# Kernel tuning notes

Hardware: AMD Instinct MI355X
Metric: run time of the kernel (lower is better)

The kernel has to match this reference:

```python
import jax, jax.numpy as jnp
import numpy as np

D_STATE = 32

def _layernorm(x, g, b, eps=1e-5):
    m = jnp.mean(x, -1, keepdims=True)
    v = jnp.mean((x - m) ** 2, -1, keepdims=True)
    return (x - m) * jax.lax.rsqrt(v + eps) * g + b

def _mlp(x, W1, b1, W2, b2):
    return jax.nn.relu(x @ W1 + b1) @ W2 + b2

def _mamba_block(x, Win, Wconv, bconv, Wxproj, Wdt, bdt, Alog, Dp, Wout):
    Bsz, T, _ = x.shape
    d_inner = Wconv.shape[0]
    dt_rank = Wdt.shape[0]
    xz = x @ Win                                   # [B,T,2*d_inner]
    xi, res = jnp.split(xz, 2, axis=-1)
    K = Wconv.shape[1]
    xp = jnp.pad(xi, ((0, 0), (K - 1, 0), (0, 0)))  # causal depthwise conv
    xi = sum(xp[:, k:k + T, :] * Wconv[:, k] for k in range(K)) + bconv
    xi = jax.nn.silu(xi)
    xdbl = xi @ Wxproj                              # [B,T,dt_rank+2*ds]
    dtr = xdbl[..., :dt_rank]
    Bm = xdbl[..., dt_rank:dt_rank + D_STATE]
    Cm = xdbl[..., dt_rank + D_STATE:]
    dt = jax.nn.softplus(dtr @ Wdt + bdt)           # [B,T,d_inner]
    A = -jnp.exp(Alog)                              # [d_inner, ds]

    def step(h, inp):
        dt_t, B_t, C_t, x_t = inp                   # [B,di],[B,ds],[B,ds],[B,di]
        dA = jnp.exp(dt_t[:, :, None] * A)          # [B,di,ds]
        dBx = (dt_t * x_t)[:, :, None] * B_t[:, None, :]
        h = dA * h + dBx
        return h, jnp.einsum('bds,bs->bd', h, C_t)

    h0 = jnp.zeros((Bsz, d_inner, D_STATE), xi.dtype)
    _, ys = jax.lax.scan(step, h0, (jnp.swapaxes(dt, 0, 1), jnp.swapaxes(Bm, 0, 1),
                                    jnp.swapaxes(Cm, 0, 1), jnp.swapaxes(xi, 0, 1)))
    y = jnp.swapaxes(ys, 0, 1) + xi * Dp
    y = y * jax.nn.silu(res)
    return y @ Wout

def _dynamics(z, Win, Wconv, bconv, Wxproj, Wdt, bdt, Alog, Dp, Wout, gamma, beta):
    out = z
    for i in range(Win.shape[0]):  # 2 stacked residual Mamba blocks
        out = out + _mamba_block(out, Win[i], Wconv[i], bconv[i], Wxproj[i],
                                 Wdt[i], bdt[i], Alog[i], Dp[i], Wout[i])
    return _layernorm(out, gamma, beta)

def setup_inputs():
    key = jax.random.key(0)
    Bz, T, IN, D, DI, DTR, K, NB = 8, 1024, 32, 64, 128, 4, 4, 2
    ks = iter(jax.random.split(key, 32))
    n = lambda shape, s=0.02: jax.random.normal(next(ks), shape, jnp.float32) * s
    return {
        'x': jax.random.normal(next(ks), (Bz, T, IN), jnp.float32),
        'We1': n((IN, 64)), 'be1': jnp.zeros((64,)),
        'We2': n((64, D)), 'be2': jnp.zeros((D,)),
        'Wd1': n((D, 64)), 'bd1': jnp.zeros((64,)),
        'Wd2': n((64, IN)), 'bd2': jnp.zeros((IN,)),
        'Win': n((NB, D, 2 * DI)),
        'Wconv': n((NB, DI, K), 0.1), 'bconv': jnp.zeros((NB, DI)),
        'Wxproj': n((NB, DI, DTR + 2 * D_STATE)),
        'Wdt': n((NB, DTR, DI), 0.1), 'bdt': jnp.full((NB, DI), -4.0),
        'Alog': jnp.tile(jnp.log(jnp.arange(1.0, 33.0)), (NB, DI, 1)),
        'Dparam': jnp.ones((NB, DI)),
        'Wout': n((NB, DI, D)),
        'gamma': jnp.ones((D,)), 'beta': jnp.zeros((D,)),
        'pred_len': 4,
    }

def reference(x, We1, be1, We2, be2, Wd1, bd1, Wd2, bd2, Win, Wconv, bconv,
              Wxproj, Wdt, bdt, Alog, Dparam, Wout, gamma, beta, pred_len):
    z = _mlp(x, We1, be1, We2, be2)
    x_rec = _mlp(z, Wd1, bd1, Wd2, bd2)
    dyn = lambda u: _dynamics(u, Win, Wconv, bconv, Wxproj, Wdt, bdt,
                              Alog, Dparam, Wout, gamma, beta)
    z_dyn = dyn(z)
    x_dyn = _mlp(z_dyn, Wd1, bd1, Wd2, bd2)
    x_pred = None
    if pred_len > 0:
        T = z.shape[1]
        curr = z
        preds = []
        for _ in range(pred_len):
            z_next = dyn(curr[:, -T:, :])[:, -1:, :]
            preds.append(z_next)
            curr = jnp.concatenate([curr, z_next], axis=1)
        x_pred = _mlp(jnp.concatenate(preds, axis=1), Wd1, bd1, Wd2, bd2)
    return (x_rec, x_dyn, x_pred, z, z_dyn)
```

## Files before the change

kernel.cpp:

```cpp
#include <hip/hip_runtime.h>

#define BSZ 8
#define TLEN 1024
#define DM 64
#define DI 128
#define DS 32
#define NCHUNK 16
#define CLEN 64
#define GEXT 1028

__device__ __forceinline__ float siluf(float x) { return x / (1.f + expf(-x)); }
__device__ __forceinline__ float softplusf(float x) { return (x > 20.f) ? x : log1pf(expf(x)); }

__global__ __launch_bounds__(256) void enc_xrec_kernel(
    const float* __restrict__ x,
    const float* __restrict__ We1, const float* __restrict__ be1,
    const float* __restrict__ We2, const float* __restrict__ be2,
    const float* __restrict__ Wd1, const float* __restrict__ bd1,
    const float* __restrict__ Wd2, const float* __restrict__ bd2,
    float* __restrict__ z, float* __restrict__ x_rec)
{
  __shared__ float s_x[16*32];
  __shared__ float s_h1[16*64];
  __shared__ float s_z[16*64];
  __shared__ float s_h2[16*64];
  const int tid = threadIdx.x;
  const int t0 = blockIdx.x * 16;
  s_x[tid]       = x[(size_t)t0*32 + tid];
  s_x[tid + 256] = x[(size_t)t0*32 + tid + 256];
  __syncthreads();
  const int j = tid & 63, tg = tid >> 6;
  {
    float w[32];
    #pragma unroll
    for (int k = 0; k < 32; k++) w[k] = We1[k*64 + j];
    #pragma unroll
    for (int q = 0; q < 4; q++) {
      int t = tg*4 + q;
      float a = be1[j];
      #pragma unroll
      for (int k = 0; k < 32; k++) a = fmaf(s_x[t*32 + k], w[k], a);
      s_h1[t*64 + j] = fmaxf(a, 0.f);
    }
  }
  __syncthreads();
  {
    float w[64];
    #pragma unroll
    for (int k = 0; k < 64; k++) w[k] = We2[k*64 + j];
    #pragma unroll
    for (int q = 0; q < 4; q++) {
      int t = tg*4 + q;
      float a = be2[j];
      #pragma unroll
      for (int k = 0; k < 64; k++) a = fmaf(s_h1[t*64 + k], w[k], a);
      s_z[t*64 + j] = a;
      z[(size_t)(t0 + t)*64 + j] = a;
    }
  }
  __syncthreads();
  {
    float w[64];
    #pragma unroll
    for (int k = 0; k < 64; k++) w[k] = Wd1[k*64 + j];
    #pragma unroll
    for (int q = 0; q < 4; q++) {
      int t = tg*4 + q;
      float a = bd1[j];
      #pragma unroll
      for (int k = 0; k < 64; k++) a = fmaf(s_z[t*64 + k], w[k], a);
      s_h2[t*64 + j] = fmaxf(a, 0.f);
    }
  }
  __syncthreads();
  {
    const int c = tid & 31, tg2 = tid >> 5;
    float w[64];
    #pragma unroll
    for (int k = 0; k < 64; k++) w[k] = Wd2[k*32 + c];
    #pragma unroll
    for (int q = 0; q < 2; q++) {
      int t = tg2*2 + q;
      float a = bd2[c];
      #pragma unroll
      for (int k = 0; k < 64; k++) a = fmaf(s_h2[t*64 + k], w[k], a);
      x_rec[(size_t)(t0 + t)*32 + c] = a;
    }
  }
}

__global__ __launch_bounds__(256) void dec2_kernel(
    const float* __restrict__ za, const float* __restrict__ zb,
    const float* __restrict__ W1, const float* __restrict__ b1,
    const float* __restrict__ W2, const float* __restrict__ b2,
    float* __restrict__ outa, float* __restrict__ outb)
{
  __shared__ float s_z[16*64];
  __shared__ float s_h[16*64];
  const int tid = threadIdx.x;
  const float* src; float* dst; int t0;
  if (blockIdx.x < 512) { src = za; dst = outa; t0 = blockIdx.x * 16; }
  else                  { src = zb; dst = outb; t0 = (blockIdx.x - 512) * 16; }
  #pragma unroll
  for (int u = 0; u < 4; u++) s_z[tid + u*256] = src[(size_t)t0*64 + tid + u*256];
  __syncthreads();
  const int j = tid & 63, tg = tid >> 6;
  {
    float w[64];
    #pragma unroll
    for (int k = 0; k < 64; k++) w[k] = W1[k*64 + j];
    #pragma unroll
    for (int q = 0; q < 4; q++) {
      int t = tg*4 + q;
      float a = b1[j];
      #pragma unroll
      for (int k = 0; k < 64; k++) a = fmaf(s_z[t*64 + k], w[k], a);
      s_h[t*64 + j] = fmaxf(a, 0.f);
    }
  }
  __syncthreads();
  {
    const int c = tid & 31, tg2 = tid >> 5;
    float w[64];
    #pragma unroll
    for (int k = 0; k < 64; k++) w[k] = W2[k*32 + c];
    #pragma unroll
    for (int q = 0; q < 2; q++) {
      int t = tg2*2 + q;
      float a = b2[c];
      #pragma unroll
      for (int k = 0; k < 64; k++) a = fmaf(s_h[t*64 + k], w[k], a);
      dst[(size_t)(t0 + t)*32 + c] = a;
    }
  }
}

__global__ __launch_bounds__(256,4) void pre_kernel(
    const float* __restrict__ in, int in_stride,
    const float* __restrict__ Win, const float* __restrict__ Wconv, const float* __restrict__ bconv,
    const float* __restrict__ Wxproj, const float* __restrict__ Wdt, const float* __restrict__ bdt,
    float* __restrict__ xibuf, float* __restrict__ resgbuf,
    float2* __restrict__ ddbuf, float* __restrict__ Bbuf, float* __restrict__ Cbuf,
    float* __restrict__ xzout)
{
  __shared__ float s_xi[8*128];
  __shared__ float s_dtr[8*4];
  const int tid = threadIdx.x;
  const int b  = blockIdx.x >> 7;
  const int t0 = (blockIdx.x & 127) * 8;

  const float* rowp[11];
  #pragma unroll
  for (int r = 0; r < 11; r++) {
    int tg = t0 - 3 + r;
    rowp[r] = (tg >= 0) ? in + ((size_t)b*in_stride + tg)*DM : in;
  }

  float acc[11];
  #pragma unroll
  for (int r = 0; r < 11; r++) acc[r] = 0.f;

  if (t0 > 0) {
    #pragma unroll
    for (int k4 = 0; k4 < 16; k4++) {
      float w0 = Win[(k4*4+0)*256 + tid];
      float w1 = Win[(k4*4+1)*256 + tid];
      float w2 = Win[(k4*4+2)*256 + tid];
      float w3 = Win[(k4*4+3)*256 + tid];
      #pragma unroll
      for (int r = 0; r < 11; r++) {
        float4 xv = *(const float4*)(rowp[r] + k4*4);
        acc[r] = fmaf(xv.x, w0, acc[r]);
        acc[r] = fmaf(xv.y, w1, acc[r]);
        acc[r] = fmaf(xv.z, w2, acc[r]);
        acc[r] = fmaf(xv.w, w3, acc[r]);
      }
    }
  } else {
    #pragma unroll
    for (int k4 = 0; k4 < 16; k4++) {
      float w0 = Win[(k4*4+0)*256 + tid];
      float w1 = Win[(k4*4+1)*256 + tid];
      float w2 = Win[(k4*4+2)*256 + tid];
      float w3 = Win[(k4*4+3)*256 + tid];
      #pragma unroll
      for (int r = 3; r < 11; r++) {
        float4 xv = *(const float4*)(rowp[r] + k4*4);
        acc[r] = fmaf(xv.x, w0, acc[r]);
        acc[r] = fmaf(xv.y, w1, acc[r]);
        acc[r] = fmaf(xv.z, w2, acc[r]);
        acc[r] = fmaf(xv.w, w3, acc[r]);
      }
    }
  }

  if (tid < 128) {
    float4 wc = *(const float4*)&Wconv[tid*4];
    float bc = bconv[tid];
    #pragma unroll
    for (int tau = 0; tau < 8; tau++) {
      float v = bc;
      v = fmaf(acc[tau+0], wc.x, v);
      v = fmaf(acc[tau+1], wc.y, v);
      v = fmaf(acc[tau+2], wc.z, v);
      v = fmaf(acc[tau+3], wc.w, v);
      float xiv = siluf(v);
      s_xi[tau*128 + tid] = xiv;
      xibuf[((size_t)b*TLEN + t0 + tau)*DI + tid] = xiv;
      xzout[((size_t)b*GEXT + t0 + tau)*128 + tid] = acc[tau+3];
    }
  } else {
    int d = tid - 128;
    #pragma unroll
    for (int tau = 0; tau < 8; tau++)
      resgbuf[((size_t)b*TLEN + t0 + tau)*DI + d] = siluf(acc[tau+3]);
  }
  __syncthreads();
  {
    const int wv = tid >> 6, c = tid & 63;
    float a0 = 0.f, a1 = 0.f;
    const float4* x0 = (const float4*)&s_xi[(wv*2+0)*128];
    const float4* x1 = (const float4*)&s_xi[(wv*2+1)*128];
    #pragma unroll 4
    for (int k4 = 0; k4 < 32; k4++) {
      float wq0 = Wxproj[(k4*4+0)*68 + 4 + c];
      float wq1 = Wxproj[(k4*4+1)*68 + 4 + c];
      float wq2 = Wxproj[(k4*4+2)*68 + 4 + c];
      float wq3 = Wxproj[(k4*4+3)*68 + 4 + c];
      float4 v0 = x0[k4], v1 = x1[k4];
      a0 = fmaf(v0.x,wq0, fmaf(v0.y,wq1, fmaf(v0.z,wq2, fmaf(v0.w,wq3, a0))));
      a1 = fmaf(v1.x,wq0, fmaf(v1.y,wq1, fmaf(v1.z,wq2, fmaf(v1.w,wq3, a1))));
    }
    size_t tb = (size_t)b*TLEN + t0 + wv*2;
    if (c < 32) {
      Bbuf[(tb+0)*DS + c] = a0; Bbuf[(tb+1)*DS + c] = a1;
    } else {
      int cc = c - 32;
      Cbuf[(tb+0)*DS + cc] = a0; Cbuf[(tb+1)*DS + cc] = a1;
    }
  }
  if (tid < 32) {
    int tau = tid >> 2, cc = tid & 3;
    float a = 0.f;
    const float4* xx = (const float4*)&s_xi[tau*128];
    #pragma unroll 4
    for (int k4 = 0; k4 < 32; k4++) {
      float4 v = xx[k4];
      a = fmaf(v.x, Wxproj[(k4*4+0)*68 + cc], a);
      a = fmaf(v.y, Wxproj[(k4*4+1)*68 + cc], a);
      a = fmaf(v.z, Wxproj[(k4*4+2)*68 + cc], a);
      a = fmaf(v.w, Wxproj[(k4*4+3)*68 + cc], a);
    }
    s_dtr[tau*4 + cc] = a;
  }
  __syncthreads();
  #pragma unroll
  for (int u = 0; u < 4; u++) {
    int i = tid + u*256;
    int tau = i >> 7, d = i & 127;
    float a = bdt[d];
    #pragma unroll
    for (int r = 0; r < 4; r++) a = fmaf(s_dtr[tau*4 + r], Wdt[r*128 + d], a);
    float dtv = softplusf(a);
    ddbuf[((size_t)b*TLEN + t0 + tau)*DI + d] = make_float2(dtv, dtv * s_xi[i]);
  }
}

#define BSWZ(row3) (((row3)&3)<<1)

__device__ __forceinline__ int xcd_wid_4096() {
  return (blockIdx.x >> 3) | ((blockIdx.x & 7) << 9);
}

__global__ __launch_bounds__(128) void scan1_kernel(
    const float2* __restrict__ ddbuf, const float* __restrict__ Bbuf,
    const float* __restrict__ Alog, float2* __restrict__ hc)
{
  __shared__ float2 s_dd[4][CLEN];
  __shared__ float  s_Bt[32][68];
  const int tid = threadIdx.x;
  const int ch = tid >> 5, s = tid & 31;
  const int wid = xcd_wid_4096();
  const int dg = wid & 31;
  const int c  = (wid >> 5) & 15;
  const int b  = wid >> 9;
  const int d0 = dg * 4;
  const float A = -__expf(Alog[(d0 + ch)*DS + s]);
  const float2* ddg = ddbuf + ((size_t)b*TLEN + c*CLEN)*DI + d0;
  const float*  Bg  = Bbuf  + ((size_t)b*TLEN + c*CLEN)*DS;
  {
    int t = tid >> 1, half = tid & 1;
    float4 rdd = *(const float4*)((const float*)(ddg + (size_t)t*DI) + half*4);
    s_dd[2*half+0][t] = make_float2(rdd.x, rdd.y);
    s_dd[2*half+1][t] = make_float2(rdd.z, rdd.w);
    #pragma unroll
    for (int j = 0; j < 4; j++) {
      int q = tid + 128*j; int tt = q >> 3, k4 = q & 7;
      float4 rB = *(const float4*)(Bg + tt*DS + k4*4);
      int cp = (((tt>>2) ^ BSWZ(k4>>1)) << 2) + (tt & 3);
      s_Bt[k4*4+0][cp] = rB.x; s_Bt[k4*4+1][cp] = rB.y;
      s_Bt[k4*4+2][cp] = rB.z; s_Bt[k4*4+3][cp] = rB.w;
    }
  }
  __syncthreads();
  float h = 0.f, dts = 0.f;
  const float4* dd4 = (const float4*)&s_dd[ch][0];
  const float4* bt4 = (const float4*)&s_Bt[s][0];
  const int swr = BSWZ(s>>3);
  #pragma unroll
  for (int j = 0; j < 8; j++) {
    float4 e0 = dd4[4*j+0], e1 = dd4[4*j+1], e2 = dd4[4*j+2], e3 = dd4[4*j+3];
    float4 bb0 = bt4[(2*j)^swr], bb1 = bt4[(2*j+1)^swr];
    h = fmaf(__expf(e0.x*A), h, e0.y*bb0.x);
    h = fmaf(__expf(e0.z*A), h, e0.w*bb0.y);
    h = fmaf(__expf(e1.x*A), h, e1.y*bb0.z);
    h = fmaf(__expf(e1.z*A), h, e1.w*bb0.w);
    h = fmaf(__expf(e2.x*A), h, e2.y*bb1.x);
    h = fmaf(__expf(e2.z*A), h, e2.w*bb1.y);
    h = fmaf(__expf(e3.x*A), h, e3.y*bb1.z);
    h = fmaf(__expf(e3.z*A), h, e3.w*bb1.w);
    dts += (e0.x + e0.z) + (e1.x + e1.z) + (e2.x + e2.z) + (e3.x + e3.z);
  }
  int o = ((b*NCHUNK + c)*DI + d0 + ch)*DS + s;
  hc[o] = make_float2(h, __expf(A*dts));
}

__global__ __launch_bounds__(128) void scan3_kernel(
    const float2* __restrict__ ddbuf, const float* __restrict__ Bbuf, const float* __restrict__ Cbuf,
    const float* __restrict__ Alog, const float2* __restrict__ hc, float* __restrict__ ysbuf,
    float* __restrict__ hout)
{
  __shared__ float2 s_dd[4][CLEN];
  __shared__ float  s_Bt[32][68];
  __shared__ float  s_Ct[32][68];
  __shared__ float  s_p[128][33];
  const int tid = threadIdx.x;
  const int ch = tid >> 5, s = tid & 31;
  const int wid = xcd_wid_4096();
  const int dg = wid & 31;
  const int c  = (wid >> 5) & 15;
  const int b  = wid >> 9;
  const int d0 = dg * 4;
  const float A = -__expf(Alog[(d0 + ch)*DS + s]);
  const float2* ddg = ddbuf + ((size_t)b*TLEN + c*CLEN)*DI + d0;
  const float*  Bg  = Bbuf  + ((size_t)b*TLEN + c*CLEN)*DS;
  const float*  Cg  = Cbuf  + ((size_t)b*TLEN + c*CLEN)*DS;

  const int ob = (d0 + ch)*DS + s;
  float2 v[15];
  #pragma unroll
  for (int q = 0; q < 15; q++) v[q] = hc[(size_t)(b*NCHUNK + q)*4096 + ob];

  {
    int t = tid >> 1, half = tid & 1;
    float4 rdd = *(const float4*)((const float*)(ddg + (size_t)t*DI) + half*4);
    s_dd[2*half+0][t] = make_float2(rdd.x, rdd.y);
    s_dd[2*half+1][t] = make_float2(rdd.z, rdd.w);
    #pragma unroll
    for (int j = 0; j < 4; j++) {
      int q = tid + 128*j; int tt = q >> 3, k4 = q & 7;
      float4 rB = *(const float4*)(Bg + tt*DS + k4*4);
      float4 rC = *(const float4*)(Cg + tt*DS + k4*4);
      int cp = (((tt>>2) ^ BSWZ(k4>>1)) << 2) + (tt & 3);
      s_Bt[k4*4+0][cp] = rB.x; s_Bt[k4*4+1][cp] = rB.y;
      s_Bt[k4*4+2][cp] = rB.z; s_Bt[k4*4+3][cp] = rB.w;
      s_Ct[k4*4+0][cp] = rC.x; s_Ct[k4*4+1][cp] = rC.y;
      s_Ct[k4*4+2][cp] = rC.z; s_Ct[k4*4+3][cp] = rC.w;
    }
  }
  float h = 0.f;
  #pragma unroll
  for (int q = 0; q < 15; q++)
    if (q < c) h = fmaf(v[q].y, h, v[q].x);
  __syncthreads();

  const float4* dd4 = (const float4*)&s_dd[ch][0];
  const float4* bt4 = (const float4*)&s_Bt[s][0];
  const float4* ct4 = (const float4*)&s_Ct[s][0];
  const int swr = BSWZ(s>>3);
  float* pr = &s_p[tid][0];
  #pragma unroll
  for (int half = 0; half < 2; half++) {
    #pragma unroll
    for (int j = 0; j < 4; j++) {
      const int jj = half*4 + j;
      float4 e0 = dd4[4*jj+0], e1 = dd4[4*jj+1], e2 = dd4[4*jj+2], e3 = dd4[4*jj+3];
      float4 bb0 = bt4[(2*jj)^swr], bb1 = bt4[(2*jj+1)^swr];
      float4 cc0 = ct4[(2*jj)^swr], cc1 = ct4[(2*jj+1)^swr];
      h = fmaf(__expf(e0.x*A), h, e0.y*bb0.x); pr[8*j+0] = h*cc0.x;
      h = fmaf(__expf(e0.z*A), h, e0.w*bb0.y); pr[8*j+1] = h*cc0.y;
      h = fmaf(__expf(e1.x*A), h, e1.y*bb0.z); pr[8*j+2] = h*cc0.z;
      h = fmaf(__expf(e1.z*A), h, e1.w*bb0.w); pr[8*j+3] = h*cc0.w;
      h = fmaf(__expf(e2.x*A), h, e2.y*bb1.x); pr[8*j+4] = h*cc1.x;
      h = fmaf(__expf(e2.z*A), h, e2.w*bb1.y); pr[8*j+5] = h*cc1.y;
      h = fmaf(__expf(e3.x*A), h, e3.y*bb1.z); pr[8*j+6] = h*cc1.z;
      h = fmaf(__expf(e3.z*A), h, e3.w*bb1.w); pr[8*j+7] = h*cc1.w;
    }
    __syncthreads();
    {
      const int ch2 = tid & 3;
      const int tq  = tid >> 2;
      float a = 0.f;
      #pragma unroll
      for (int s2 = 0; s2 < 32; s2++) a += s_p[ch2*32 + s2][tq];
      ysbuf[(size_t)(b*TLEN + c*CLEN + half*32 + tq)*DI + d0 + ch2] = a;
    }
    __syncthreads();
  }
  if (c == 15) hout[(size_t)(b*DI + d0 + ch)*DS + s] = h;
}

__global__ __launch_bounds__(256,4) void post_kernel(
    const float* __restrict__ ysbuf, const float* __restrict__ xibuf, const float* __restrict__ resgbuf,
    const float* __restrict__ Dp, const float* __restrict__ Wout,
    const float* __restrict__ basebuf, int base_stride,
    float* __restrict__ curg, float* __restrict__ zdyn, float* __restrict__ predz,
    const float* __restrict__ gamma, const float* __restrict__ beta, int mode)
{
  __shared__ float s_y[8*128];
  const int tid = threadIdx.x;
  const int b  = blockIdx.x >> 7;
  const int t0 = (blockIdx.x & 127) * 8;
  #pragma unroll
  for (int u = 0; u < 4; u++) {
    int i = tid + u*256;
    size_t g = (size_t)(b*TLEN + t0)*DI + i;
    s_y[i] = (ysbuf[g] + xibuf[g]*Dp[i & 127]) * resgbuf[g];
  }
  __syncthreads();
  #pragma unroll
  for (int u = 0; u < 2; u++) {
    int i = tid + u*256;
    int tau = i >> 6, c = i & 63;
    float a = 0.f;
    const float4* yy = (const float4*)&s_y[tau*128];
    #pragma unroll 4
    for (int k4 = 0; k4 < 32; k4++) {
      float4 vv = yy[k4];
      a = fmaf(vv.x, Wout[(k4*4+0)*64 + c], a);
      a = fmaf(vv.y, Wout[(k4*4+1)*64 + c], a);
      a = fmaf(vv.z, Wout[(k4*4+2)*64 + c], a);
      a = fmaf(vv.w, Wout[(k4*4+3)*64 + c], a);
    }
    float base = basebuf[((size_t)b*base_stride + t0 + tau)*DM + c];
    float val = base + a;
    if (mode == 0) {
      curg[((size_t)b*GEXT + t0 + tau)*DM + c] = val;
    } else {
      float sum = val;
      #pragma unroll
      for (int m = 1; m < 64; m <<= 1) sum += __shfl_xor(sum, m);
      float mean = sum * (1.f/64.f);
      float dv = val - mean;
      float vs = dv*dv;
      #pragma unroll
      for (int m = 1; m < 64; m <<= 1) vs += __shfl_xor(vs, m);
      float oln = dv * rsqrtf(vs*(1.f/64.f) + 1e-5f) * gamma[c] + beta[c];
      zdyn[(size_t)(b*TLEN + t0 + tau)*DM + c] = oln;
      if (t0 + tau == TLEN-1) predz[(size_t)(b*4 + 0)*DM + c] = oln;
    }
  }
}

__device__ __forceinline__ void mamba_token(
    int tid, int b, int gn, const float* __restrict__ s_in,
    float* __restrict__ xzg, float* __restrict__ hbuf,
    const float* __restrict__ Win, const float* __restrict__ Wcv, const float* __restrict__ bcv,
    const float* __restrict__ Wxp, const float* __restrict__ Wdt, const float* __restrict__ bdt,
    const float* __restrict__ Al, const float* __restrict__ Dpp, const float* __restrict__ Wo,
    float* __restrict__ s_xz, float* __restrict__ s_xi, float* __restrict__ s_rg,
    float* __restrict__ s_dt, float* __restrict__ s_B, float* __restrict__ s_C,
    float* __restrict__ s_dtr, float* __restrict__ s_yp, float* __restrict__ s_y,
    float* __restrict__ s_ssm)
{
  {
    float a = 0.f;
    #pragma unroll
    for (int k = 0; k < 64; k++) a = fmaf(s_in[k], Win[k*256 + tid], a);
    s_xz[tid] = a;
  }
  __syncthreads();
  if (tid < 128) {
    xzg[((size_t)b*GEXT + gn)*128 + tid] = s_xz[tid];
    float acc = bcv[tid];
    acc = fmaf(xzg[((size_t)b*GEXT + gn-3)*128 + tid], Wcv[tid*4+0], acc);
    acc = fmaf(xzg[((size_t)b*GEXT + gn-2)*128 + tid], Wcv[tid*4+1], acc);
    acc = fmaf(xzg[((size_t)b*GEXT + gn-1)*128 + tid], Wcv[tid*4+2], acc);
    acc = fmaf(s_xz[tid], Wcv[tid*4+3], acc);
    s_xi[tid] = siluf(acc);
    s_rg[tid] = siluf(s_xz[128 + tid]);
  }
  __syncthreads();
  if (tid < 68) {
    float a = 0.f;
    #pragma unroll 4
    for (int k = 0; k < 128; k++) a = fmaf(s_xi[k], Wxp[k*68 + tid], a);
    if (tid < 4)       s_dtr[tid] = a;
    else if (tid < 36) s_B[tid-4] = a;
    else               s_C[tid-36] = a;
  }
  __syncthreads();
  if (tid < 128) {
    float a = bdt[tid];
    #pragma unroll
    for (int r = 0; r < 4; r++) a = fmaf(s_dtr[r], Wdt[r*128 + tid], a);
    s_dt[tid] = softplusf(a);
  }
  __syncthreads();
  {
    int d = tid >> 1, sh = (tid & 1) * 16;
    float dtd = s_dt[d], dtxd = dtd * s_xi[d];
    float yp = 0.f;
    #pragma unroll
    for (int q = 0; q < 16; q++) {
      int s = sh + q;
      size_t oo = (size_t)(b*DI + d)*DS + s;
      float A = -__expf(Al[d*DS + s]);
      float h = hbuf[oo];
      h = fmaf(__expf(dtd*A), h, dtxd*s_B[s]);
      hbuf[oo] = h;
      yp = fmaf(s_C[s], h, yp);
    }
    s_yp[(tid & 1)*128 + d] = yp;
  }
  __syncthreads();
  if (tid < 128) s_y[tid] = ((s_yp[tid] + s_yp[128 + tid]) + s_xi[tid]*Dpp[tid]) * s_rg[tid];
  __syncthreads();
  if (tid < 64) {
    float a = 0.f;
    #pragma unroll 4
    for (int k = 0; k < 128; k++) a = fmaf(s_y[k], Wo[k*64 + tid], a);
    s_ssm[tid] = a;
  }
  __syncthreads();
}

__global__ __launch_bounds__(256) void ext2_kernel(
    int p,
    float* __restrict__ predz, float* __restrict__ curg,
    float* __restrict__ xz0, float* __restrict__ xz1,
    float* __restrict__ hbuf0, float* __restrict__ hbuf1,
    const float* __restrict__ Win0, const float* __restrict__ Wcv0, const float* __restrict__ bcv0,
    const float* __restrict__ Wxp0, const float* __restrict__ Wdt0, const float* __restrict__ bdt0,
    const float* __restrict__ Al0, const float* __restrict__ Dp0, const float* __restrict__ Wo0,
    const float* __restrict__ Win1, const float* __restrict__ Wcv1, const float* __restrict__ bcv1,
    const float* __restrict__ Wxp1, const float* __restrict__ Wdt1, const float* __restrict__ bdt1,
    const float* __restrict__ Al1, const float* __restrict__ Dp1, const float* __restrict__ Wo1,
    const float* __restrict__ gamma, const float* __restrict__ beta)
{
  __shared__ float s_in[64], s_cg[64], s_ssm[64];
  __shared__ float s_xz[256], s_yp[256];
  __shared__ float s_xi[128], s_rg[128], s_dt[128], s_y[128];
  __shared__ float s_B[32], s_C[32], s_dtr[4];
  const int tid = threadIdx.x;
  const int b = blockIdx.x;
  const int gn = 1023 + p;

  if (tid < 64) s_in[tid] = predz[(size_t)(b*4 + p-1)*DM + tid];
  __syncthreads();
  mamba_token(tid, b, gn, s_in, xz0, hbuf0, Win0, Wcv0, bcv0, Wxp0, Wdt0, bdt0,
              Al0, Dp0, Wo0, s_xz, s_xi, s_rg, s_dt, s_B, s_C, s_dtr, s_yp, s_y, s_ssm);
  if (tid < 64) {
    float cg = s_in[tid] + s_ssm[tid];
    curg[((size_t)b*GEXT + gn)*DM + tid] = cg;
    s_cg[tid] = cg;
  }
  __syncthreads();
  if (tid < 64) s_in[tid] = s_cg[tid];
  __syncthreads();
  mamba_token(tid, b, gn, s_in, xz1, hbuf1, Win1, Wcv1, bcv1, Wxp1, Wdt1, bdt1,
              Al1, Dp1, Wo1, s_xz, s_xi, s_rg, s_dt, s_B, s_C, s_dtr, s_yp, s_y, s_ssm);
  if (tid < 64) {
    float val = s_cg[tid] + s_ssm[tid];
    float sum = val;
    #pragma unroll
    for (int m = 1; m < 64; m <<= 1) sum += __shfl_xor(sum, m);
    float mean = sum * (1.f/64.f);
    float dv = val - mean;
    float vs = dv*dv;
    #pragma unroll
    for (int m = 1; m < 64; m <<= 1) vs += __shfl_xor(vs, m);
    float oln = dv * rsqrtf(vs*(1.f/64.f) + 1e-5f) * gamma[tid] + beta[tid];
    predz[(size_t)(b*4 + p)*DM + tid] = oln;
  }
}

extern "C" void kernel_launch(void* const* d_in, const int* in_sizes, int n_in,
                              void* d_out, int out_size, void* d_ws, size_t ws_size,
                              hipStream_t stream)
{
  (void)in_sizes; (void)n_in; (void)out_size; (void)ws_size;
  const float* x     = (const float*)d_in[0];
  const float* We1   = (const float*)d_in[1];
  const float* be1   = (const float*)d_in[2];
  const float* We2   = (const float*)d_in[3];
  const float* be2   = (const float*)d_in[4];
  const float* Wd1   = (const float*)d_in[5];
  const float* bd1   = (const float*)d_in[6];
  const float* Wd2   = (const float*)d_in[7];
  const float* bd2   = (const float*)d_in[8];
  const float* Win   = (const float*)d_in[9];
  const float* Wconv = (const float*)d_in[10];
  const float* bconv = (const float*)d_in[11];
  const float* Wxp   = (const float*)d_in[12];
  const float* Wdt   = (const float*)d_in[13];
  const float* bdt   = (const float*)d_in[14];
  const float* Alog  = (const float*)d_in[15];
  const float* Dp    = (const float*)d_in[16];
  const float* Wout  = (const float*)d_in[17];
  const float* gamma = (const float*)d_in[18];
  const float* beta  = (const float*)d_in[19];

  float* o      = (float*)d_out;
  float* x_rec  = o;
  float* x_dyn  = o + 262144;
  float* x_pred = o + 524288;
  float* z      = o + 525312;
  float* zdyn   = o + 1049600;

  float* w      = (float*)d_ws;
  float* xi0    = w;
  float* resg0  = xi0   + 1048576;
  float2* dd0   = (float2*)(resg0 + 1048576);
  float* Bb0    = resg0 + 1048576 + 2097152;
  float* Cb0    = Bb0   + 262144;
  float* xi1    = Cb0   + 262144;
  float* resg1  = xi1   + 1048576;
  float2* dd1   = (float2*)(resg1 + 1048576);
  float* Bb1    = resg1 + 1048576 + 2097152;
  float* Cb1    = Bb1   + 262144;
  float* ys     = Cb1   + 262144;
  float2* hc    = (float2*)(ys + 1048576);
  float* predz  = ys + 1048576 + 1048576;
  float* xz0    = predz + 2048;
  float* xz1    = xz0   + 1052672;
  float* curg   = xz1   + 1052672;
  float* hbuf0  = curg  + 526336;
  float* hbuf1  = hbuf0 + 32768;

  const float* Win0 = Win,   *Win1 = Win + 64*256;
  const float* Wcv0 = Wconv, *Wcv1 = Wconv + 128*4;
  const float* bcv0 = bconv, *bcv1 = bconv + 128;
  const float* Wxp0 = Wxp,   *Wxp1 = Wxp + 128*68;
  const float* Wdt0 = Wdt,   *Wdt1 = Wdt + 4*128;
  const float* bdt0 = bdt,   *bdt1 = bdt + 128;
  const float* Al0  = Alog,  *Al1  = Alog + 128*32;
  const float* Dp0  = Dp,    *Dp1  = Dp + 128;
  const float* Wo0  = Wout,  *Wo1  = Wout + 128*64;

  enc_xrec_kernel<<<dim3(512), dim3(256), 0, stream>>>(x, We1, be1, We2, be2, Wd1, bd1, Wd2, bd2, z, x_rec);

  pre_kernel<<<dim3(1024), dim3(256), 0, stream>>>(z, TLEN,
                                                   Win0, Wcv0, bcv0, Wxp0, Wdt0, bdt0,
                                                   xi0, resg0, dd0, Bb0, Cb0, xz0);
  scan1_kernel<<<dim3(4096), dim3(128), 0, stream>>>(dd0, Bb0, Al0, hc);
  scan3_kernel<<<dim3(4096), dim3(128), 0, stream>>>(dd0, Bb0, Cb0, Al0, hc, ys, hbuf0);
  post_kernel<<<dim3(1024), dim3(256), 0, stream>>>(ys, xi0, resg0, Dp0, Wo0,
                                                    z, TLEN, curg,
                                                    (float*)nullptr, (float*)nullptr,
                                                    (const float*)nullptr, (const float*)nullptr, 0);

  pre_kernel<<<dim3(1024), dim3(256), 0, stream>>>(curg, GEXT,
                                                   Win1, Wcv1, bcv1, Wxp1, Wdt1, bdt1,
                                                   xi1, resg1, dd1, Bb1, Cb1, xz1);
  scan1_kernel<<<dim3(4096), dim3(128), 0, stream>>>(dd1, Bb1, Al1, hc);
  scan3_kernel<<<dim3(4096), dim3(128), 0, stream>>>(dd1, Bb1, Cb1, Al1, hc, ys, hbuf1);
  post_kernel<<<dim3(1024), dim3(256), 0, stream>>>(ys, xi1, resg1, Dp1, Wo1,
                                                    curg, GEXT, (float*)nullptr,
                                                    zdyn, predz, gamma, beta, 1);

  for (int p = 1; p <= 3; p++) {
    ext2_kernel<<<dim3(8), dim3(256), 0, stream>>>(p, predz, curg, xz0, xz1, hbuf0, hbuf1,
        Win0, Wcv0, bcv0, Wxp0, Wdt0, bdt0, Al0, Dp0, Wo0,
        Win1, Wcv1, bcv1, Wxp1, Wdt1, bdt1, Al1, Dp1, Wo1,
        gamma, beta);
  }

  dec2_kernel<<<dim3(514), dim3(256), 0, stream>>>(zdyn, predz, Wd1, bd1, Wd2, bd2, x_dyn, x_pred);
}
```

Baseline: 242.3 us.

## Fuse decoder MLP into post kernel and merge prediction steps into one kernel

The x_dyn decoder MLP now runs inside the second post_kernel on the layernormed tokens already held in shared memory, so the separate dec2 kernel and its re-read of zdyn go away. The three per-step ext2 launches become one ext_all_kernel that loops over prediction steps, keeps predicted tokens in shared memory, and decodes x_pred at the end. This cuts five launches to two fewer kernels and removes global round trips. In exchange post_kernel uses more shared memory and registers, which could lower occupancy, and the x_pred decode runs on only 8 blocks.

```diff
diff --git a/kernel.cpp b/kernel.cpp
--- a/kernel.cpp
+++ b/kernel.cpp
@@ -85,52 +85,6 @@
       #pragma unroll
       for (int k = 0; k < 64; k++) a = fmaf(s_h2[t*64 + k], w[k], a);
       x_rec[(size_t)(t0 + t)*32 + c] = a;
-    }
-  }
-}
-
-__global__ __launch_bounds__(256) void dec2_kernel(
-    const float* __restrict__ za, const float* __restrict__ zb,
-    const float* __restrict__ W1, const float* __restrict__ b1,
-    const float* __restrict__ W2, const float* __restrict__ b2,
-    float* __restrict__ outa, float* __restrict__ outb)
-{
-  __shared__ float s_z[16*64];
-  __shared__ float s_h[16*64];
-  const int tid = threadIdx.x;
-  const float* src; float* dst; int t0;
-  if (blockIdx.x < 512) { src = za; dst = outa; t0 = blockIdx.x * 16; }
-  else                  { src = zb; dst = outb; t0 = (blockIdx.x - 512) * 16; }
-  #pragma unroll
-  for (int u = 0; u < 4; u++) s_z[tid + u*256] = src[(size_t)t0*64 + tid + u*256];
-  __syncthreads();
-  const int j = tid & 63, tg = tid >> 6;
-  {
-    float w[64];
-    #pragma unroll
-    for (int k = 0; k < 64; k++) w[k] = W1[k*64 + j];
-    #pragma unroll
-    for (int q = 0; q < 4; q++) {
-      int t = tg*4 + q;
-      float a = b1[j];
-      #pragma unroll
-      for (int k = 0; k < 64; k++) a = fmaf(s_z[t*64 + k], w[k], a);
-      s_h[t*64 + j] = fmaxf(a, 0.f);
-    }
-  }
-  __syncthreads();
-  {
-    const int c = tid & 31, tg2 = tid >> 5;
-    float w[64];
-    #pragma unroll
-    for (int k = 0; k < 64; k++) w[k] = W2[k*32 + c];
-    #pragma unroll
-    for (int q = 0; q < 2; q++) {
-      int t = tg2*2 + q;
-      float a = b2[c];
-      #pragma unroll
-      for (int k = 0; k < 64; k++) a = fmaf(s_h[t*64 + k], w[k], a);
-      dst[(size_t)(t0 + t)*32 + c] = a;
     }
   }
 }
@@ -415,9 +369,14 @@
     const float* __restrict__ Dp, const float* __restrict__ Wout,
     const float* __restrict__ basebuf, int base_stride,
     float* __restrict__ curg, float* __restrict__ zdyn, float* __restrict__ predz,
-    const float* __restrict__ gamma, const float* __restrict__ beta, int mode)
+    const float* __restrict__ gamma, const float* __restrict__ beta,
+    const float* __restrict__ Wd1, const float* __restrict__ bd1,
+    const float* __restrict__ Wd2, const float* __restrict__ bd2,
+    float* __restrict__ xdyn, int mode)
 {
   __shared__ float s_y[8*128];
+  __shared__ float s_z[8*64];
+  __shared__ float s_h[8*64];
   const int tid = threadIdx.x;
   const int b  = blockIdx.x >> 7;
   const int t0 = (blockIdx.x & 127) * 8;
@@ -457,7 +416,42 @@
       for (int m = 1; m < 64; m <<= 1) vs += __shfl_xor(vs, m);
       float oln = dv * rsqrtf(vs*(1.f/64.f) + 1e-5f) * gamma[c] + beta[c];
       zdyn[(size_t)(b*TLEN + t0 + tau)*DM + c] = oln;
+      s_z[tau*64 + c] = oln;
       if (t0 + tau == TLEN-1) predz[(size_t)(b*4 + 0)*DM + c] = oln;
+    }
+  }
+  if (mode == 1) {
+    __syncthreads();
+    #pragma unroll
+    for (int u = 0; u < 2; u++) {
+      int i = tid + u*256;
+      int t = i >> 6, j = i & 63;
+      float a = bd1[j];
+      const float4* zz = (const float4*)&s_z[t*64];
+      #pragma unroll 4
+      for (int k4 = 0; k4 < 16; k4++) {
+        float4 zv = zz[k4];
+        a = fmaf(zv.x, Wd1[(k4*4+0)*64 + j], a);
+        a = fmaf(zv.y, Wd1[(k4*4+1)*64 + j], a);
+        a = fmaf(zv.z, Wd1[(k4*4+2)*64 + j], a);
+        a = fmaf(zv.w, Wd1[(k4*4+3)*64 + j], a);
+      }
+      s_h[i] = fmaxf(a, 0.f);
+    }
+    __syncthreads();
+    {
+      int t = tid >> 5, c = tid & 31;
+      float a = bd2[c];
+      const float4* hh = (const float4*)&s_h[t*64];
+      #pragma unroll 4
+      for (int k4 = 0; k4 < 16; k4++) {
+        float4 hv = hh[k4];
+        a = fmaf(hv.x, Wd2[(k4*4+0)*32 + c], a);
+        a = fmaf(hv.y, Wd2[(k4*4+1)*32 + c], a);
+        a = fmaf(hv.z, Wd2[(k4*4+2)*32 + c], a);
+        a = fmaf(hv.w, Wd2[(k4*4+3)*32 + c], a);
+      }
+      xdyn[(size_t)(b*TLEN + t0 + t)*32 + c] = a;
     }
   }
 }
@@ -535,8 +529,7 @@
   __syncthreads();
 }
 
-__global__ __launch_bounds__(256) void ext2_kernel(
-    int p,
+__global__ __launch_bounds__(256) void ext_all_kernel(
     float* __restrict__ predz, float* __restrict__ curg,
     float* __restrict__ xz0, float* __restrict__ xz1,
     float* __restrict__ hbuf0, float* __restrict__ hbuf1,
@@ -546,42 +539,83 @@
     const float* __restrict__ Win1, const float* __restrict__ Wcv1, const float* __restrict__ bcv1,
     const float* __restrict__ Wxp1, const float* __restrict__ Wdt1, const float* __restrict__ bdt1,
     const float* __restrict__ Al1, const float* __restrict__ Dp1, const float* __restrict__ Wo1,
-    const float* __restrict__ gamma, const float* __restrict__ beta)
+    const float* __restrict__ gamma, const float* __restrict__ beta,
+    const float* __restrict__ Wd1, const float* __restrict__ bd1,
+    const float* __restrict__ Wd2, const float* __restrict__ bd2,
+    float* __restrict__ x_pred)
 {
   __shared__ float s_in[64], s_cg[64], s_ssm[64];
   __shared__ float s_xz[256], s_yp[256];
   __shared__ float s_xi[128], s_rg[128], s_dt[128], s_y[128];
   __shared__ float s_B[32], s_C[32], s_dtr[4];
+  __shared__ float s_pz[4][64];
+  __shared__ float s_h[4][64];
   const int tid = threadIdx.x;
   const int b = blockIdx.x;
-  const int gn = 1023 + p;
-
-  if (tid < 64) s_in[tid] = predz[(size_t)(b*4 + p-1)*DM + tid];
-  __syncthreads();
-  mamba_token(tid, b, gn, s_in, xz0, hbuf0, Win0, Wcv0, bcv0, Wxp0, Wdt0, bdt0,
-              Al0, Dp0, Wo0, s_xz, s_xi, s_rg, s_dt, s_B, s_C, s_dtr, s_yp, s_y, s_ssm);
-  if (tid < 64) {
-    float cg = s_in[tid] + s_ssm[tid];
-    curg[((size_t)b*GEXT + gn)*DM + tid] = cg;
-    s_cg[tid] = cg;
-  }
-  __syncthreads();
-  if (tid < 64) s_in[tid] = s_cg[tid];
-  __syncthreads();
-  mamba_token(tid, b, gn, s_in, xz1, hbuf1, Win1, Wcv1, bcv1, Wxp1, Wdt1, bdt1,
-              Al1, Dp1, Wo1, s_xz, s_xi, s_rg, s_dt, s_B, s_C, s_dtr, s_yp, s_y, s_ssm);
-  if (tid < 64) {
-    float val = s_cg[tid] + s_ssm[tid];
-    float sum = val;
-    #pragma unroll
-    for (int m = 1; m < 64; m <<= 1) sum += __shfl_xor(sum, m);
-    float mean = sum * (1.f/64.f);
-    float dv = val - mean;
-    float vs = dv*dv;
-    #pragma unroll
-    for (int m = 1; m < 64; m <<= 1) vs += __shfl_xor(vs, m);
-    float oln = dv * rsqrtf(vs*(1.f/64.f) + 1e-5f) * gamma[tid] + beta[tid];
-    predz[(size_t)(b*4 + p)*DM + tid] = oln;
+
+  if (tid < 64) s_pz[0][tid] = predz[(size_t)(b*4 + 0)*DM + tid];
+  __syncthreads();
+
+  for (int p = 1; p <= 3; p++) {
+    const int gn = 1023 + p;
+    if (tid < 64) s_in[tid] = s_pz[p-1][tid];
+    __syncthreads();
+    mamba_token(tid, b, gn, s_in, xz0, hbuf0, Win0, Wcv0, bcv0, Wxp0, Wdt0, bdt0,
+                Al0, Dp0, Wo0, s_xz, s_xi, s_rg, s_dt, s_B, s_C, s_dtr, s_yp, s_y, s_ssm);
+    if (tid < 64) {
+      float cg = s_in[tid] + s_ssm[tid];
+      curg[((size_t)b*GEXT + gn)*DM + tid] = cg;
+      s_cg[tid] = cg;
+      s_in[tid] = cg;
+    }
+    __syncthreads();
+    mamba_token(tid, b, gn, s_in, xz1, hbuf1, Win1, Wcv1, bcv1, Wxp1, Wdt1, bdt1,
+                Al1, Dp1, Wo1, s_xz, s_xi, s_rg, s_dt, s_B, s_C, s_dtr, s_yp, s_y, s_ssm);
+    if (tid < 64) {
+      float val = s_cg[tid] + s_ssm[tid];
+      float sum = val;
+      #pragma unroll
+      for (int m = 1; m < 64; m <<= 1) sum += __shfl_xor(sum, m);
+      float mean = sum * (1.f/64.f);
+      float dv = val - mean;
+      float vs = dv*dv;
+      #pragma unroll
+      for (int m = 1; m < 64; m <<= 1) vs += __shfl_xor(vs, m);
+      float oln = dv * rsqrtf(vs*(1.f/64.f) + 1e-5f) * gamma[tid] + beta[tid];
+      predz[(size_t)(b*4 + p)*DM + tid] = oln;
+      s_pz[p][tid] = oln;
+    }
+    __syncthreads();
+  }
+
+  {
+    int t = tid >> 6, j = tid & 63;
+    float a = bd1[j];
+    const float4* zz = (const float4*)&s_pz[t][0];
+    #pragma unroll 4
+    for (int k4 = 0; k4 < 16; k4++) {
+      float4 zv = zz[k4];
+      a = fmaf(zv.x, Wd1[(k4*4+0)*64 + j], a);
+      a = fmaf(zv.y, Wd1[(k4*4+1)*64 + j], a);
+      a = fmaf(zv.z, Wd1[(k4*4+2)*64 + j], a);
+      a = fmaf(zv.w, Wd1[(k4*4+3)*64 + j], a);
+    }
+    s_h[t][j] = fmaxf(a, 0.f);
+  }
+  __syncthreads();
+  if (tid < 128) {
+    int t = tid >> 5, c = tid & 31;
+    float a = bd2[c];
+    const float4* hh = (const float4*)&s_h[t][0];
+    #pragma unroll 4
+    for (int k4 = 0; k4 < 16; k4++) {
+      float4 hv = hh[k4];
+      a = fmaf(hv.x, Wd2[(k4*4+0)*32 + c], a);
+      a = fmaf(hv.y, Wd2[(k4*4+1)*32 + c], a);
+      a = fmaf(hv.z, Wd2[(k4*4+2)*32 + c], a);
+      a = fmaf(hv.w, Wd2[(k4*4+3)*32 + c], a);
+    }
+    x_pred[(size_t)(b*4 + t)*32 + c] = a;
   }
 }
 
@@ -658,7 +692,10 @@
   post_kernel<<<dim3(1024), dim3(256), 0, stream>>>(ys, xi0, resg0, Dp0, Wo0,
                                                     z, TLEN, curg,
                                                     (float*)nullptr, (float*)nullptr,
-                                                    (const float*)nullptr, (const float*)nullptr, 0);
+                                                    (const float*)nullptr, (const float*)nullptr,
+                                                    (const float*)nullptr, (const float*)nullptr,
+                                                    (const float*)nullptr, (const float*)nullptr,
+                                                    (float*)nullptr, 0);
 
   pre_kernel<<<dim3(1024), dim3(256), 0, stream>>>(curg, GEXT,
                                                    Win1, Wcv1, bcv1, Wxp1, Wdt1, bdt1,
@@ -667,14 +704,11 @@
   scan3_kernel<<<dim3(4096), dim3(128), 0, stream>>>(dd1, Bb1, Cb1, Al1, hc, ys, hbuf1);
   post_kernel<<<dim3(1024), dim3(256), 0, stream>>>(ys, xi1, resg1, Dp1, Wo1,
                                                     curg, GEXT, (float*)nullptr,
-                                                    zdyn, predz, gamma, beta, 1);
-
-  for (int p = 1; p <= 3; p++) {
-    ext2_kernel<<<dim3(8), dim3(256), 0, stream>>>(p, predz, curg, xz0, xz1, hbuf0, hbuf1,
-        Win0, Wcv0, bcv0, Wxp0, Wdt0, bdt0, Al0, Dp0, Wo0,
-        Win1, Wcv1, bcv1, Wxp1, Wdt1, bdt1, Al1, Dp1, Wo1,
-        gamma, beta);
-  }
-
-  dec2_kernel<<<dim3(514), dim3(256), 0, stream>>>(zdyn, predz, Wd1, bd1, Wd2, bd2, x_dyn, x_pred);
-}
+                                                    zdyn, predz, gamma, beta,
+                                                    Wd1, bd1, Wd2, bd2, x_dyn, 1);
+
+  ext_all_kernel<<<dim3(8), dim3(256), 0, stream>>>(predz, curg, xz0, xz1, hbuf0, hbuf1,
+      Win0, Wcv0, bcv0, Wxp0, Wdt0, bdt0, Al0, Dp0, Wo0,
+      Win1, Wcv1, bcv1, Wxp1, Wdt1, bdt1, Al1, Dp1, Wo1,
+      gamma, beta, Wd1, bd1, Wd2, bd2, x_pred);
+}
```

Result: faster. 235.9 us (-2.6%).
